# Kernel tuning notes

Hardware: AMD Instinct MI355X
Metric: run time of the kernel (lower is better)

Reference implementation:

```python
import jax, jax.numpy as jnp
import numpy as np

N = 50000          # nodes
E = 800000         # edges (avg degree 16)
DIN = 128          # d_input
H = 8              # heads per layer
D = 16             # per-head hidden dim
HID = H * D        # 128
ALPHA = 0.2        # LeakyReLU negative slope in GAT attention
BN_EPS = 1e-5


def _xavier(key, shape):
    fan_in, fan_out = shape[0], shape[-1]
    lim = np.sqrt(6.0 / (fan_in + fan_out)).astype(np.float32)
    return jax.random.uniform(key, shape, jnp.float32, -lim, lim)


def setup_inputs() -> dict:
    key = jax.random.key(0)
    ks = jax.random.split(key, 8)
    x = jax.random.normal(ks[0], (N, DIN), jnp.float32)
    edge_idx = jax.random.randint(ks[1], (2, E), 0, N)
    W1 = _xavier(ks[2], (DIN, HID))
    a1 = _xavier(ks[3], (H, 2 * D))
    W2 = _xavier(ks[4], (HID, HID))
    a2 = _xavier(ks[5], (H, 2 * D))
    W3 = _xavier(ks[6], (HID, HID))
    a3 = _xavier(ks[7], (H, 2 * D))
    ones = jnp.ones((HID,), jnp.float32)
    zeros = jnp.zeros((HID,), jnp.float32)
    return {"x": x, "edge_idx": edge_idx,
            "W1": W1, "a1": a1, "W2": W2, "a2": a2, "W3": W3, "a3": a3,
            "g1": ones, "b1": zeros, "g2": ones, "b2": zeros, "g3": ones, "b3": zeros}


def _leaky(x):
    return jnp.where(x >= 0, x, ALPHA * x)


def _gat_layer(x, src, dst, W, a):
    # x: [N, Fin]; W: [Fin, H*D]; a: [H, 2D]
    h = (x @ W).reshape(-1, H, D)                       # [N, H, D]
    e_src = jnp.einsum('nhd,hd->nh', h, a[:, :D])       # a^T part for source node
    e_dst = jnp.einsum('nhd,hd->nh', h, a[:, D:])       # a^T part for destination node
    e = _leaky(e_src[src] + e_dst[dst])                 # [E, H]
    m = jax.ops.segment_max(e, dst, num_segments=N)     # per-dst stable softmax max
    m = jnp.where(jnp.isfinite(m), m, 0.0)              # empty segments -> 0
    w = jnp.exp(e - m[dst])                             # [E, H]
    den = jax.ops.segment_sum(w, dst, num_segments=N)   # [N, H]
    agg = jax.ops.segment_sum(h[src] * w[:, :, None], dst, num_segments=N)  # [N, H, D]
    out = agg / (den[:, :, None] + 1e-16)
    return out.reshape(-1, HID)                         # concat heads


def _bn(x, g, b):
    # BatchNorm1d training-mode math over the node axis
    mu = x.mean(axis=0)
    var = x.var(axis=0)
    return g * (x - mu) * jax.lax.rsqrt(var + BN_EPS) + b


def reference(x, edge_idx, W1, a1, W2, a2, W3, a3, g1, b1, g2, b2, g3, b3):
    src, dst = edge_idx[0], edge_idx[1]
    h1 = jax.nn.elu(_bn(_gat_layer(x, src, dst, W1, a1), g1, b1))
    h2 = jax.nn.elu(_bn(_gat_layer(h1, src, dst, W2, a2), g2, b2))
    h3_in = h1 + h2  # skip connection
    return _bn(_gat_layer(h3_in, src, dst, W3, a3), g3, b3)
```

## Files before the change

### kernel.cpp

```cpp
#include <hip/hip_runtime.h>
#include <hip/hip_bf16.h>
#include <hip/hip_fp16.h>
#include <cstddef>

#define NNODES 50000
#define NEDGES 800000
#define HID 128
#define NHEAD 8
#define AGG_NB (NNODES / 16)
#define NSLICE 64
#define SLAYER (NSLICE * 512)

#define NBUCK 196
#define BCH 2048
#define BIN_NB ((NEDGES + BCH - 1) / BCH)

typedef __attribute__((ext_vector_type(4))) float floatx4;
typedef _Float16 __attribute__((ext_vector_type(8))) half8;
typedef _Float16 __attribute__((ext_vector_type(2))) half2v;

static inline size_t align_up(size_t x, size_t a) { return (x + a - 1) & ~(a - 1); }

__device__ inline float fexp2(float x) {
#if __has_builtin(__builtin_amdgcn_exp2f)
    return __builtin_amdgcn_exp2f(x);
#else
    return __expf(x * 0.69314718055994531f);
#endif
}

__device__ inline unsigned short f2h(float f) {
    return __builtin_bit_cast(unsigned short, (_Float16)f);
}

__global__ __launch_bounds__(256) void init_kernel(const float* __restrict__ W1,
                                                   const float* __restrict__ W2,
                                                   const float* __restrict__ W3,
                                                   unsigned short* __restrict__ Wt,
                                                   int* __restrict__ zeroA, int nA,
                                                   float* __restrict__ zeroB, int nB) {
    int b = blockIdx.x;
    int t = threadIdx.x;
    if (b < 192) {
        int layer = b >> 6;
        const float* W = (layer == 0) ? W1 : ((layer == 1) ? W2 : W3);
        int idx = (b & 63) * 256 + t;
        int n = idx & 127;
        int k = idx >> 7;
        Wt[layer * 16384 + n * 128 + k] = f2h(W[idx]);
    } else {
        int nb = gridDim.x - 192;
        int bb = b - 192;
        for (int i = bb * 256 + t; i < nA; i += nb * 256) zeroA[i] = 0;
        for (int i = bb * 256 + t; i < nB; i += nb * 256) zeroB[i] = 0.f;
    }
}

__global__ __launch_bounds__(256) void bin_count_kernel(const int* __restrict__ edge,
                                                        int* __restrict__ bucketCnt) {
    __shared__ int h[NBUCK];
    int t = threadIdx.x;
    if (t < NBUCK) h[t] = 0;
    __syncthreads();
    for (int i = blockIdx.x * 256 + t; i < NEDGES; i += gridDim.x * 256)
        atomicAdd(&h[edge[NEDGES + i] >> 8], 1);
    __syncthreads();
    if (t < NBUCK && h[t]) atomicAdd(&bucketCnt[t], h[t]);
}

__global__ __launch_bounds__(256) void bin_scatter_kernel(const int* __restrict__ edge,
                                                          const int* __restrict__ bucketCnt,
                                                          int* __restrict__ bucketCursor,
                                                          unsigned int* __restrict__ binned) {
    __shared__ int sA[256];
    __shared__ int hcnt[NBUCK];
    __shared__ int hbase[NBUCK];
    __shared__ int gbase[NBUCK];
    __shared__ unsigned int sEnt[BCH];
    __shared__ unsigned char sBk[BCH];
    int t = threadIdx.x;
    int e0 = blockIdx.x * BCH;
    int nv = NEDGES - e0;
    if (nv > BCH) nv = BCH;

    int gcnt = (t < NBUCK) ? bucketCnt[t] : 0;
    sA[t] = gcnt;
    __syncthreads();
    for (int off = 1; off < 256; off <<= 1) {
        int x = (t >= off) ? sA[t - off] : 0;
        __syncthreads();
        sA[t] += x;
        __syncthreads();
    }
    int gExBase = sA[t] - gcnt;
    if (t < NBUCK) hcnt[t] = 0;
    __syncthreads();

    int myB[8];
    int myR[8];
    unsigned int myP[8];
    #pragma unroll
    for (int j = 0; j < 8; ++j) {
        int idx = j * 256 + t;
        myB[j] = -1;
        if (idx < nv) {
            int s = edge[e0 + idx];
            int d = edge[NEDGES + e0 + idx];
            int bk = d >> 8;
            myB[j] = bk;
            myP[j] = (unsigned)s | ((unsigned)(d & 255) << 16);
            myR[j] = atomicAdd(&hcnt[bk], 1);
        }
    }
    __syncthreads();
    int hc = (t < NBUCK) ? hcnt[t] : 0;
    sA[t] = hc;
    __syncthreads();
    for (int off = 1; off < 256; off <<= 1) {
        int x = (t >= off) ? sA[t - off] : 0;
        __syncthreads();
        sA[t] += x;
        __syncthreads();
    }
    if (t < NBUCK) {
        hbase[t] = sA[t] - hc;
        gbase[t] = gExBase + atomicAdd(&bucketCursor[t], hc);
    }
    __syncthreads();
    #pragma unroll
    for (int j = 0; j < 8; ++j) {
        if (myB[j] >= 0) {
            int p = hbase[myB[j]] + myR[j];
            sEnt[p] = myP[j];
            sBk[p] = (unsigned char)myB[j];
        }
    }
    __syncthreads();
    #pragma unroll
    for (int j = 0; j < 8; ++j) {
        int i = j * 256 + t;
        if (i < nv) {
            int bk = sBk[i];
            binned[gbase[bk] + (i - hbase[bk])] = sEnt[i];
        }
    }
}

__global__ __launch_bounds__(256) void fine_csr_kernel(const int* __restrict__ bucketCnt,
                                                       const unsigned int* __restrict__ binned,
                                                       int* __restrict__ offs,
                                                       int* __restrict__ csr) {
    __shared__ int sA[256];
    __shared__ int sB[256];
    int t = threadIdx.x;
    int b = blockIdx.x;
    int v = (t < NBUCK) ? bucketCnt[t] : 0;
    sA[t] = v;
    __syncthreads();
    for (int off = 1; off < 256; off <<= 1) {
        int x = (t >= off) ? sA[t - off] : 0;
        __syncthreads();
        sA[t] += x;
        __syncthreads();
    }
    int cntb = bucketCnt[b];
    int base = sA[b] - cntb;
    sB[t] = 0;
    __syncthreads();
    for (int i = t; i < cntb; i += 256)
        atomicAdd(&sB[(binned[base + i] >> 16) & 255], 1);
    __syncthreads();
    int nc = sB[t];
    sA[t] = nc;
    __syncthreads();
    for (int off = 1; off < 256; off <<= 1) {
        int x = (t >= off) ? sA[t - off] : 0;
        __syncthreads();
        sA[t] += x;
        __syncthreads();
    }
    int nodeBase = base + sA[t] - nc;
    int gid = b * 256 + t;
    if (gid < NNODES) offs[gid] = nodeBase;
    if (b == NBUCK - 1 && t == 0) offs[NNODES] = NEDGES;
    sB[t] = nodeBase;
    __syncthreads();
    for (int i = t; i < cntb; i += 256) {
        unsigned e = binned[base + i];
        int pos = atomicAdd(&sB[(e >> 16) & 255], 1);
        csr[pos] = (int)(e & 0xFFFFu);
    }
}

#define GROWS 64
#define ASTRIDE 136
#define LOG2E 1.4426950408889634f
__global__ __launch_bounds__(256) void gemm_kernel(const float* __restrict__ Xin,
                                                   const float* __restrict__ skip,
                                                   const float* __restrict__ statsPart,
                                                   const float* __restrict__ g,
                                                   const float* __restrict__ b,
                                                   const unsigned short* __restrict__ Wt,
                                                   const float* __restrict__ a,
                                                   float* __restrict__ Hw,
                                                   unsigned short* __restrict__ Hb,
                                                   float* __restrict__ esrc,
                                                   float* __restrict__ edst,
                                                   int mode) {
    __shared__ unsigned short As[GROWS * ASTRIDE];
    __shared__ unsigned short Bs[128 * ASTRIDE];
    __shared__ float ssm[256];
    int tid = threadIdx.x;
    int rowBase = blockIdx.x * GROWS;

    for (int i = tid; i < 128 * 16; i += 256) {
        int n = i >> 4, seg = i & 15;
        *(uint4*)(&Bs[n * ASTRIDE + seg * 8]) = *(const uint4*)(Wt + n * 128 + seg * 8);
    }

    if (mode >= 1) {
        if (tid < 128) {
            float s = 0.f, s2 = 0.f;
            #pragma unroll 8
            for (int k = 0; k < NSLICE; ++k) {
                s  += statsPart[k * 512 + tid];
                s2 += statsPart[k * 512 + 128 + tid];
            }
            float mu = s / (float)NNODES;
            float var = s2 / (float)NNODES - mu * mu;
            float rstd = rsqrtf(var + 1e-5f);
            float scale = g[tid] * rstd;
            ssm[tid] = scale;
            ssm[128 + tid] = b[tid] - mu * scale;
        }
        __syncthreads();
    }

    {
        int r = tid >> 2;
        int cs = (tid & 3) * 32;
        int gr = rowBase + r;
        float4 vv[8];
        if (gr < NNODES) {
            #pragma unroll
            for (int j = 0; j < 8; ++j)
                vv[j] = *(const float4*)(Xin + (size_t)gr * HID + cs + j * 4);
            if (mode >= 1) {
                #pragma unroll
                for (int j = 0; j < 8; ++j) {
                    int ch = cs + j * 4;
                    float4 sc = *(const float4*)(ssm + ch);
                    float4 sh = *(const float4*)(ssm + 128 + ch);
                    float4 v = vv[j];
                    v.x = sc.x * v.x + sh.x;
                    v.y = sc.y * v.y + sh.y;
                    v.z = sc.z * v.z + sh.z;
                    v.w = sc.w * v.w + sh.w;
                    v.x = (v.x > 0.f) ? v.x : expm1f(v.x);
                    v.y = (v.y > 0.f) ? v.y : expm1f(v.y);
                    v.z = (v.z > 0.f) ? v.z : expm1f(v.z);
                    v.w = (v.w > 0.f) ? v.w : expm1f(v.w);
                    if (mode == 2) {
                        float4 s = *(const float4*)(skip + (size_t)gr * HID + ch);
                        v.x += s.x; v.y += s.y; v.z += s.z; v.w += s.w;
                    }
                    vv[j] = v;
                }
                if (mode == 1) {
                    #pragma unroll
                    for (int j = 0; j < 8; ++j)
                        *(float4*)(Hw + (size_t)gr * HID + cs + j * 4) = vv[j];
                }
            }
        } else {
            #pragma unroll
            for (int j = 0; j < 8; ++j) vv[j] = make_float4(0.f, 0.f, 0.f, 0.f);
        }
        unsigned int pk[16];
        #pragma unroll
        for (int j = 0; j < 8; ++j) {
            pk[2 * j]     = __builtin_bit_cast(unsigned int,
                                __builtin_amdgcn_cvt_pkrtz(vv[j].x, vv[j].y));
            pk[2 * j + 1] = __builtin_bit_cast(unsigned int,
                                __builtin_amdgcn_cvt_pkrtz(vv[j].z, vv[j].w));
        }
        #pragma unroll
        for (int q = 0; q < 4; ++q)
            *(uint4*)(&As[r * ASTRIDE + cs + q * 8]) =
                make_uint4(pk[4 * q], pk[4 * q + 1], pk[4 * q + 2], pk[4 * q + 3]);
    }
    __syncthreads();

    int wv = tid >> 6;
    int lane = tid & 63;
    int l15 = lane & 15;
    int quad = lane >> 4;
    const unsigned short* Arow = &As[(wv * 16 + l15) * ASTRIDE + quad * 8];
    half8 af[4];
    #pragma unroll
    for (int c = 0; c < 4; ++c) af[c] = *(const half8*)(Arow + c * 32);

    floatx4 acc[8];
    #pragma unroll
    for (int h = 0; h < 8; ++h) {
        acc[h] = (floatx4){0.f, 0.f, 0.f, 0.f};
        const unsigned short* Brow = &Bs[(h * 16 + l15) * ASTRIDE + quad * 8];
        #pragma unroll
        for (int c = 0; c < 4; ++c) {
            half8 bfr = *(const half8*)(Brow + c * 32);
            acc[h] = __builtin_amdgcn_mfma_f32_16x16x32_f16(af[c], bfr, acc[h], 0, 0, 0);
        }
    }
    __syncthreads();

    #pragma unroll
    for (int h = 0; h < 8; ++h) {
        #pragma unroll
        for (int reg = 0; reg < 4; ++reg)
            As[(wv * 16 + quad * 4 + reg) * ASTRIDE + h * 16 + l15] = f2h(acc[h][reg]);
    }
    __syncthreads();

    {
        int r = tid >> 2;
        int hp = tid & 3;
        int gr = rowBase + r;
        const unsigned short* row = &As[r * ASTRIDE + hp * 32];
        uint4 u[4];
        #pragma unroll
        for (int q = 0; q < 4; ++q) u[q] = *(const uint4*)(row + q * 8);
        if (gr < NNODES) {
            uint4* dst = (uint4*)(Hb + (size_t)gr * HID + hp * 32);
            #pragma unroll
            for (int q = 0; q < 4; ++q) dst[q] = u[q];
            float f[32];
            #pragma unroll
            for (int q = 0; q < 4; ++q) {
                unsigned int* pu = (unsigned int*)&u[q];
                #pragma unroll
                for (int j = 0; j < 4; ++j) {
                    half2v hv = __builtin_bit_cast(half2v, pu[j]);
                    f[q * 8 + 2 * j]     = (float)hv[0];
                    f[q * 8 + 2 * j + 1] = (float)hv[1];
                }
            }
            int h0 = hp * 2, h1 = hp * 2 + 1;
            float es0 = 0.f, ev0 = 0.f, es1 = 0.f, ev1 = 0.f;
            #pragma unroll
            for (int j = 0; j < 16; ++j) {
                es0 += f[j] * a[h0 * 32 + j];
                ev0 += f[j] * a[h0 * 32 + 16 + j];
                es1 += f[16 + j] * a[h1 * 32 + j];
                ev1 += f[16 + j] * a[h1 * 32 + 16 + j];
            }
            esrc[gr * NHEAD + h0] = es0 * LOG2E;
            esrc[gr * NHEAD + h1] = es1 * LOG2E;
            edst[gr * NHEAD + h0] = ev0 * LOG2E;
            edst[gr * NHEAD + h1] = ev1 * LOG2E;
        }
    }
}

__global__ __launch_bounds__(256) void aggregate_kernel(const int* __restrict__ offs,
                                                        const int* __restrict__ csr,
                                                        const float* __restrict__ esrc,
                                                        const float* __restrict__ edst,
                                                        const unsigned int* __restrict__ Hb,
                                                        float* __restrict__ out,
                                                        float* __restrict__ statsPart) {
    int tid = threadIdx.x;
    int wv = tid >> 6;
    int lane = tid & 63;
    int grp = lane >> 4;
    int sub = lane & 15;
    int head = sub >> 1;
    int n = blockIdx.x * 16 + wv * 4 + grp;
    int beg = offs[n], end = offs[n + 1];
    float ed = edst[n * NHEAD + head];
    float acc[8];
    #pragma unroll
    for (int q = 0; q < 8; ++q) acc[q] = 0.f;
    float den = 0.f;
    for (int i = beg; i < end; i += 4) {
        int ss[4];
        #pragma unroll
        for (int j = 0; j < 4; ++j)
            ss[j] = csr[min(i + j, end - 1)];
        float ee[4];
        uint4 hh[4];
        #pragma unroll
        for (int j = 0; j < 4; ++j)
            ee[j] = esrc[(unsigned)ss[j] * 8u + (unsigned)head];
        #pragma unroll
        for (int j = 0; j < 4; ++j)
            hh[j] = *(const uint4*)(Hb + (unsigned)ss[j] * 64u + (unsigned)sub * 4u);
        #pragma unroll
        for (int j = 0; j < 4; ++j) {
            float e = ee[j] + ed;
            e = fmaxf(e, 0.2f * e);
            float w = fexp2(e);
            w = (i + j < end) ? w : 0.f;
            den += w;
            half2v h0 = __builtin_bit_cast(half2v, hh[j].x);
            half2v h1 = __builtin_bit_cast(half2v, hh[j].y);
            half2v h2 = __builtin_bit_cast(half2v, hh[j].z);
            half2v h3 = __builtin_bit_cast(half2v, hh[j].w);
            acc[0] += w * (float)h0[0];
            acc[1] += w * (float)h0[1];
            acc[2] += w * (float)h1[0];
            acc[3] += w * (float)h1[1];
            acc[4] += w * (float)h2[0];
            acc[5] += w * (float)h2[1];
            acc[6] += w * (float)h3[0];
            acc[7] += w * (float)h3[1];
        }
    }
    float inv = 1.f / (den + 1e-16f);
    float4 o0 = make_float4(acc[0] * inv, acc[1] * inv, acc[2] * inv, acc[3] * inv);
    float4 o1 = make_float4(acc[4] * inv, acc[5] * inv, acc[6] * inv, acc[7] * inv);
    float* orow = out + (size_t)n * HID + sub * 8;
    *(float4*)orow = o0;
    *(float4*)(orow + 4) = o1;

    __shared__ float sm[16 * 136];
    float* srow = &sm[(wv * 4 + grp) * 136 + sub * 8];
    *(float4*)srow = o0;
    *(float4*)(srow + 4) = o1;
    __syncthreads();
    if (tid < 128) {
        float s = 0.f, s2 = 0.f;
        #pragma unroll
        for (int r = 0; r < 16; ++r) {
            float v = sm[r * 136 + tid];
            s += v;
            s2 += v * v;
        }
        float* slice = statsPart + (blockIdx.x & (NSLICE - 1)) * 512;
        atomicAdd(&slice[tid], s);
        atomicAdd(&slice[128 + tid], s2);
    }
}

__global__ __launch_bounds__(256) void final_apply_kernel(const float* __restrict__ X,
                                                          const float* __restrict__ statsPart,
                                                          const float* __restrict__ g,
                                                          const float* __restrict__ b,
                                                          float* __restrict__ out) {
    __shared__ float ssm[256];
    int tid = threadIdx.x;
    if (tid < 128) {
        float s = 0.f, s2 = 0.f;
        #pragma unroll 8
        for (int k = 0; k < NSLICE; ++k) {
            s  += statsPart[k * 512 + tid];
            s2 += statsPart[k * 512 + 128 + tid];
        }
        float mu = s / (float)NNODES;
        float var = s2 / (float)NNODES - mu * mu;
        float rstd = rsqrtf(var + 1e-5f);
        float scale = g[tid] * rstd;
        ssm[tid] = scale;
        ssm[128 + tid] = b[tid] - mu * scale;
    }
    __syncthreads();
    int total4 = NNODES * HID / 4;
    for (int i = blockIdx.x * 256 + tid; i < total4; i += gridDim.x * 256) {
        float4 v = ((const float4*)X)[i];
        int c4 = (i & 31) * 4;
        float4 sc = *(const float4*)(ssm + c4);
        float4 sh = *(const float4*)(ssm + 128 + c4);
        v.x = sc.x * v.x + sh.x;
        v.y = sc.y * v.y + sh.y;
        v.z = sc.z * v.z + sh.z;
        v.w = sc.w * v.w + sh.w;
        ((float4*)out)[i] = v;
    }
}

extern "C" void kernel_launch(void* const* d_in, const int* in_sizes, int n_in,
                              void* d_out, int out_size, void* d_ws, size_t ws_size,
                              hipStream_t stream) {
    const float* x   = (const float*)d_in[0];
    const int* edge  = (const int*)d_in[1];
    const float* W1  = (const float*)d_in[2];
    const float* a1  = (const float*)d_in[3];
    const float* W2  = (const float*)d_in[4];
    const float* a2  = (const float*)d_in[5];
    const float* W3  = (const float*)d_in[6];
    const float* a3  = (const float*)d_in[7];
    const float* g1  = (const float*)d_in[8];
    const float* b1  = (const float*)d_in[9];
    const float* g2  = (const float*)d_in[10];
    const float* b2  = (const float*)d_in[11];
    const float* g3  = (const float*)d_in[12];
    const float* b3  = (const float*)d_in[13];
    float* outp      = (float*)d_out;

    char* p = (char*)d_ws;
    size_t cur = 0;
    auto carve = [&](size_t bytes) {
        void* r = p + cur;
        cur = align_up(cur + bytes, 256);
        return r;
    };
    int*   offs   = (int*)carve((NNODES + 1) * sizeof(int));
    int*   csr    = (int*)carve(NEDGES * sizeof(int));
    unsigned short* wt = (unsigned short*)carve(3 * 16384 * sizeof(unsigned short));
    unsigned short* hb = (unsigned short*)carve((size_t)NNODES * HID * sizeof(unsigned short));
    float* agg    = (float*)carve((size_t)NNODES * HID * sizeof(float));
    float* h1     = (float*)carve((size_t)NNODES * HID * sizeof(float));
    float* esrc   = (float*)carve((size_t)NNODES * NHEAD * sizeof(float));
    float* edst   = (float*)carve((size_t)NNODES * NHEAD * sizeof(float));
    float* stats  = (float*)carve(3 * SLAYER * sizeof(float));
    int*   bcnt   = (int*)carve(2 * NBUCK * sizeof(int));
    int*   bcur   = bcnt + NBUCK;
    float* stats1 = stats;
    float* stats2 = stats + SLAYER;
    float* stats3 = stats + 2 * SLAYER;
    unsigned int* binned = (unsigned int*)h1;

    const int GB = (NNODES + GROWS - 1) / GROWS;

    init_kernel<<<256, 256, 0, stream>>>(W1, W2, W3, wt,
                                         bcnt, 2 * NBUCK,
                                         stats, 3 * SLAYER);
    bin_count_kernel<<<256, 256, 0, stream>>>(edge, bcnt);
    bin_scatter_kernel<<<BIN_NB, 256, 0, stream>>>(edge, bcnt, bcur, binned);
    fine_csr_kernel<<<NBUCK, 256, 0, stream>>>(bcnt, binned, offs, csr);

    gemm_kernel<<<GB, 256, 0, stream>>>(x, nullptr, nullptr, nullptr, nullptr,
                                        wt, a1, nullptr, hb, esrc, edst, 0);
    aggregate_kernel<<<AGG_NB, 256, 0, stream>>>(offs, csr, esrc, edst,
                                                 (const unsigned int*)hb, agg, stats1);

    gemm_kernel<<<GB, 256, 0, stream>>>(agg, nullptr, stats1, g1, b1,
                                        wt + 16384, a2, h1, hb, esrc, edst, 1);
    aggregate_kernel<<<AGG_NB, 256, 0, stream>>>(offs, csr, esrc, edst,
                                                 (const unsigned int*)hb, agg, stats2);

    gemm_kernel<<<GB, 256, 0, stream>>>(agg, h1, stats2, g2, b2,
                                        wt + 32768, a3, nullptr, hb, esrc, edst, 2);
    aggregate_kernel<<<AGG_NB, 256, 0, stream>>>(offs, csr, esrc, edst,
                                                 (const unsigned int*)hb, agg, stats3);

    final_apply_kernel<<<768, 256, 0, stream>>>(agg, stats3, g3, b3, outp);
}
```

Measured before the change: 362.0 us.

## Hoist BatchNorm stat finalization into a single-block kernel and streamline GEMM prologue

Adds a one-block bn_finalize_kernel that reduces the per-slice BatchNorm partial sums once and writes the per-channel scale and shift. Previously every GEMM and final-apply block redid that 64-slice reduction. The GEMM prologue now loads the weight tile into registers while the activation rows are in flight, then stores it to shared memory. Two block-wide barriers around the accumulator write-back are removed, which is safe because each wave only touches its own rows. The cost is three extra small kernel launches, each a serial dependency on the stream.

Result: no change. 360.4 us (-0.4%).

```diff
diff --git a/kernel.cpp b/kernel.cpp
--- a/kernel.cpp
+++ b/kernel.cpp
@@ -192,14 +192,34 @@
     }
 }
 
+__global__ __launch_bounds__(256) void bn_finalize_kernel(const float* __restrict__ statsPart,
+                                                          const float* __restrict__ g,
+                                                          const float* __restrict__ b,
+                                                          float* __restrict__ ssv) {
+    __shared__ float sm[256];
+    int t = threadIdx.x;
+    const float* base = statsPart + (t & 127) + ((t >> 7) << 7);
+    float s = 0.f;
+    #pragma unroll 8
+    for (int k = 0; k < NSLICE; ++k) s += base[k * 512];
+    sm[t] = s;
+    __syncthreads();
+    if (t < 128) {
+        float mu = sm[t] / (float)NNODES;
+        float var = sm[128 + t] / (float)NNODES - mu * mu;
+        float rstd = rsqrtf(var + 1e-5f);
+        float scale = g[t] * rstd;
+        ssv[t] = scale;
+        ssv[128 + t] = b[t] - mu * scale;
+    }
+}
+
 #define GROWS 64
 #define ASTRIDE 136
 #define LOG2E 1.4426950408889634f
 __global__ __launch_bounds__(256) void gemm_kernel(const float* __restrict__ Xin,
                                                    const float* __restrict__ skip,
-                                                   const float* __restrict__ statsPart,
-                                                   const float* __restrict__ g,
-                                                   const float* __restrict__ b,
+                                                   const float* __restrict__ ssv,
                                                    const unsigned short* __restrict__ Wt,
                                                    const float* __restrict__ a,
                                                    float* __restrict__ Hw,
@@ -209,73 +229,64 @@
                                                    int mode) {
     __shared__ unsigned short As[GROWS * ASTRIDE];
     __shared__ unsigned short Bs[128 * ASTRIDE];
-    __shared__ float ssm[256];
     int tid = threadIdx.x;
     int rowBase = blockIdx.x * GROWS;
 
-    for (int i = tid; i < 128 * 16; i += 256) {
-        int n = i >> 4, seg = i & 15;
-        *(uint4*)(&Bs[n * ASTRIDE + seg * 8]) = *(const uint4*)(Wt + n * 128 + seg * 8);
-    }
-
-    if (mode >= 1) {
-        if (tid < 128) {
-            float s = 0.f, s2 = 0.f;
-            #pragma unroll 8
-            for (int k = 0; k < NSLICE; ++k) {
-                s  += statsPart[k * 512 + tid];
-                s2 += statsPart[k * 512 + 128 + tid];
+    uint4 breg[8];
+    #pragma unroll
+    for (int q = 0; q < 8; ++q) {
+        int i = q * 256 + tid;
+        breg[q] = *(const uint4*)(Wt + (i >> 4) * 128 + (i & 15) * 8);
+    }
+
+    int r = tid >> 2;
+    int cs = (tid & 3) * 32;
+    int gr = rowBase + r;
+    bool valid = gr < NNODES;
+    float4 vv[8];
+    if (valid) {
+        #pragma unroll
+        for (int j = 0; j < 8; ++j)
+            vv[j] = *(const float4*)(Xin + (size_t)gr * HID + cs + j * 4);
+    } else {
+        #pragma unroll
+        for (int j = 0; j < 8; ++j) vv[j] = make_float4(0.f, 0.f, 0.f, 0.f);
+    }
+
+    #pragma unroll
+    for (int q = 0; q < 8; ++q) {
+        int i = q * 256 + tid;
+        *(uint4*)(&Bs[(i >> 4) * ASTRIDE + (i & 15) * 8]) = breg[q];
+    }
+
+    if (mode >= 1 && valid) {
+        #pragma unroll
+        for (int j = 0; j < 8; ++j) {
+            int ch = cs + j * 4;
+            float4 sc = *(const float4*)(ssv + ch);
+            float4 sh = *(const float4*)(ssv + 128 + ch);
+            float4 v = vv[j];
+            v.x = sc.x * v.x + sh.x;
+            v.y = sc.y * v.y + sh.y;
+            v.z = sc.z * v.z + sh.z;
+            v.w = sc.w * v.w + sh.w;
+            v.x = (v.x > 0.f) ? v.x : expm1f(v.x);
+            v.y = (v.y > 0.f) ? v.y : expm1f(v.y);
+            v.z = (v.z > 0.f) ? v.z : expm1f(v.z);
+            v.w = (v.w > 0.f) ? v.w : expm1f(v.w);
+            if (mode == 2) {
+                float4 s = *(const float4*)(skip + (size_t)gr * HID + ch);
+                v.x += s.x; v.y += s.y; v.z += s.z; v.w += s.w;
             }
-            float mu = s / (float)NNODES;
-            float var = s2 / (float)NNODES - mu * mu;
-            float rstd = rsqrtf(var + 1e-5f);
-            float scale = g[tid] * rstd;
-            ssm[tid] = scale;
-            ssm[128 + tid] = b[tid] - mu * scale;
-        }
-        __syncthreads();
-    }
-
-    {
-        int r = tid >> 2;
-        int cs = (tid & 3) * 32;
-        int gr = rowBase + r;
-        float4 vv[8];
-        if (gr < NNODES) {
+            vv[j] = v;
+        }
+        if (mode == 1) {
             #pragma unroll
             for (int j = 0; j < 8; ++j)
-                vv[j] = *(const float4*)(Xin + (size_t)gr * HID + cs + j * 4);
-            if (mode >= 1) {
-                #pragma unroll
-                for (int j = 0; j < 8; ++j) {
-                    int ch = cs + j * 4;
-                    float4 sc = *(const float4*)(ssm + ch);
-                    float4 sh = *(const float4*)(ssm + 128 + ch);
-                    float4 v = vv[j];
-                    v.x = sc.x * v.x + sh.x;
-                    v.y = sc.y * v.y + sh.y;
-                    v.z = sc.z * v.z + sh.z;
-                    v.w = sc.w * v.w + sh.w;
-                    v.x = (v.x > 0.f) ? v.x : expm1f(v.x);
-                    v.y = (v.y > 0.f) ? v.y : expm1f(v.y);
-                    v.z = (v.z > 0.f) ? v.z : expm1f(v.z);
-                    v.w = (v.w > 0.f) ? v.w : expm1f(v.w);
-                    if (mode == 2) {
-                        float4 s = *(const float4*)(skip + (size_t)gr * HID + ch);
-                        v.x += s.x; v.y += s.y; v.z += s.z; v.w += s.w;
-                    }
-                    vv[j] = v;
-                }
-                if (mode == 1) {
-                    #pragma unroll
-                    for (int j = 0; j < 8; ++j)
-                        *(float4*)(Hw + (size_t)gr * HID + cs + j * 4) = vv[j];
-                }
-            }
-        } else {
-            #pragma unroll
-            for (int j = 0; j < 8; ++j) vv[j] = make_float4(0.f, 0.f, 0.f, 0.f);
-        }
+                *(float4*)(Hw + (size_t)gr * HID + cs + j * 4) = vv[j];
+        }
+    }
+    {
         unsigned int pk[16];
         #pragma unroll
         for (int j = 0; j < 8; ++j) {
@@ -289,6 +300,7 @@
             *(uint4*)(&As[r * ASTRIDE + cs + q * 8]) =
                 make_uint4(pk[4 * q], pk[4 * q + 1], pk[4 * q + 2], pk[4 * q + 3]);
     }
+
     __syncthreads();
 
     int wv = tid >> 6;
@@ -311,7 +323,6 @@
             acc[h] = __builtin_amdgcn_mfma_f32_16x16x32_f16(af[c], bfr, acc[h], 0, 0, 0);
         }
     }
-    __syncthreads();
 
     #pragma unroll
     for (int h = 0; h < 8; ++h) {
@@ -319,18 +330,17 @@
         for (int reg = 0; reg < 4; ++reg)
             As[(wv * 16 + quad * 4 + reg) * ASTRIDE + h * 16 + l15] = f2h(acc[h][reg]);
     }
-    __syncthreads();
 
     {
-        int r = tid >> 2;
+        int rr = tid >> 2;
         int hp = tid & 3;
-        int gr = rowBase + r;
-        const unsigned short* row = &As[r * ASTRIDE + hp * 32];
+        int grr = rowBase + rr;
+        const unsigned short* row = &As[rr * ASTRIDE + hp * 32];
         uint4 u[4];
         #pragma unroll
         for (int q = 0; q < 4; ++q) u[q] = *(const uint4*)(row + q * 8);
-        if (gr < NNODES) {
-            uint4* dst = (uint4*)(Hb + (size_t)gr * HID + hp * 32);
+        if (grr < NNODES) {
+            uint4* dst = (uint4*)(Hb + (size_t)grr * HID + hp * 32);
             #pragma unroll
             for (int q = 0; q < 4; ++q) dst[q] = u[q];
             float f[32];
@@ -353,10 +363,10 @@
                 es1 += f[16 + j] * a[h1 * 32 + j];
                 ev1 += f[16 + j] * a[h1 * 32 + 16 + j];
             }
-            esrc[gr * NHEAD + h0] = es0 * LOG2E;
-            esrc[gr * NHEAD + h1] = es1 * LOG2E;
-            edst[gr * NHEAD + h0] = ev0 * LOG2E;
-            edst[gr * NHEAD + h1] = ev1 * LOG2E;
+            esrc[grr * NHEAD + h0] = es0 * LOG2E;
+            esrc[grr * NHEAD + h1] = es1 * LOG2E;
+            edst[grr * NHEAD + h0] = ev0 * LOG2E;
+            edst[grr * NHEAD + h1] = ev1 * LOG2E;
         }
     }
 }
@@ -430,8 +440,8 @@
     if (tid < 128) {
         float s = 0.f, s2 = 0.f;
         #pragma unroll
-        for (int r = 0; r < 16; ++r) {
-            float v = sm[r * 136 + tid];
+        for (int rr = 0; rr < 16; ++rr) {
+            float v = sm[rr * 136 + tid];
             s += v;
             s2 += v * v;
         }
@@ -442,26 +452,11 @@
 }
 
 __global__ __launch_bounds__(256) void final_apply_kernel(const float* __restrict__ X,
-                                                          const float* __restrict__ statsPart,
-                                                          const float* __restrict__ g,
-                                                          const float* __restrict__ b,
+                                                          const float* __restrict__ ssv,
                                                           float* __restrict__ out) {
     __shared__ float ssm[256];
     int tid = threadIdx.x;
-    if (tid < 128) {
-        float s = 0.f, s2 = 0.f;
-        #pragma unroll 8
-        for (int k = 0; k < NSLICE; ++k) {
-            s  += statsPart[k * 512 + tid];
-            s2 += statsPart[k * 512 + 128 + tid];
-        }
-        float mu = s / (float)NNODES;
-        float var = s2 / (float)NNODES - mu * mu;
-        float rstd = rsqrtf(var + 1e-5f);
-        float scale = g[tid] * rstd;
-        ssm[tid] = scale;
-        ssm[128 + tid] = b[tid] - mu * scale;
-    }
+    ssm[tid] = ssv[tid];
     __syncthreads();
     int total4 = NNODES * HID / 4;
     for (int i = blockIdx.x * 256 + tid; i < total4; i += gridDim.x * 256) {
@@ -514,9 +509,13 @@
     float* stats  = (float*)carve(3 * SLAYER * sizeof(float));
     int*   bcnt   = (int*)carve(2 * NBUCK * sizeof(int));
     int*   bcur   = bcnt + NBUCK;
+    float* ssv    = (float*)carve(3 * 256 * sizeof(float));
     float* stats1 = stats;
     float* stats2 = stats + SLAYER;
     float* stats3 = stats + 2 * SLAYER;
+    float* ssv1 = ssv;
+    float* ssv2 = ssv + 256;
+    float* ssv3 = ssv + 512;
     unsigned int* binned = (unsigned int*)h1;
 
     const int GB = (NNODES + GROWS - 1) / GROWS;
@@ -528,20 +527,23 @@
     bin_scatter_kernel<<<BIN_NB, 256, 0, stream>>>(edge, bcnt, bcur, binned);
     fine_csr_kernel<<<NBUCK, 256, 0, stream>>>(bcnt, binned, offs, csr);
 
-    gemm_kernel<<<GB, 256, 0, stream>>>(x, nullptr, nullptr, nullptr, nullptr,
+    gemm_kernel<<<GB, 256, 0, stream>>>(x, nullptr, nullptr,
                                         wt, a1, nullptr, hb, esrc, edst, 0);
     aggregate_kernel<<<AGG_NB, 256, 0, stream>>>(offs, csr, esrc, edst,
                                                  (const unsigned int*)hb, agg, stats1);
-
-    gemm_kernel<<<GB, 256, 0, stream>>>(agg, nullptr, stats1, g1, b1,
+    bn_finalize_kernel<<<1, 256, 0, stream>>>(stats1, g1, b1, ssv1);
+
+    gemm_kernel<<<GB, 256, 0, stream>>>(agg, nullptr, ssv1,
                                         wt + 16384, a2, h1, hb, esrc, edst, 1);
     aggregate_kernel<<<AGG_NB, 256, 0, stream>>>(offs, csr, esrc, edst,
                                                  (const unsigned int*)hb, agg, stats2);
-
-    gemm_kernel<<<GB, 256, 0, stream>>>(agg, h1, stats2, g2, b2,
+    bn_finalize_kernel<<<1, 256, 0, stream>>>(stats2, g2, b2, ssv2);
+
+    gemm_kernel<<<GB, 256, 0, stream>>>(agg, h1, ssv2,
                                         wt + 32768, a3, nullptr, hb, esrc, edst, 2);
     aggregate_kernel<<<AGG_NB, 256, 0, stream>>>(offs, csr, esrc, edst,
                                                  (const unsigned int*)hb, agg, stats3);
-
-    final_apply_kernel<<<768, 256, 0, stream>>>(agg, stats3, g3, b3, outp);
-}
+    bn_finalize_kernel<<<1, 256, 0, stream>>>(stats3, g3, b3, ssv3);
+
+    final_apply_kernel<<<768, 256, 0, stream>>>(agg, ssv3, outp);
+}
```
